# Performance work log

Hardware: AMD Instinct MI355X
Metric: run time of the kernel (lower is better)

The kernel has to match this reference:

```python
import jax, jax.numpy as jnp
import numpy as np

QMAX = 127.0  # 8-bit symmetric: levels in [-128, 127]


def _ste_round(v):
    # round with straight-through estimator (matches torch fake-quant training)
    return v + jax.lax.stop_gradient(jnp.round(v) - v)


def _act_fake_quant(x, clip_factor):
    # per-tensor symmetric fake quant with learnable clip (lac):
    # clip range = sigmoid(clip_factor) * max|x|
    scale = jax.nn.sigmoid(clip_factor) * jnp.max(jnp.abs(x)) / QMAX
    return jnp.clip(_ste_round(x / scale), -QMAX - 1.0, QMAX) * scale


def _weight_fake_quant(w):
    # per-output-channel symmetric fake quant; w: [out, in]
    scale = jnp.max(jnp.abs(w), axis=1, keepdims=True) / QMAX
    return jnp.clip(_ste_round(w / scale), -QMAX - 1.0, QMAX) * scale


def setup_inputs() -> dict:
    key = jax.random.key(0)
    k1, k2, k3, k4 = jax.random.split(key, 4)
    B, S, H, I = 8, 8192, 1024, 2816
    return {
        "x": jax.random.normal(k1, (B, S, H), dtype=jnp.float32),
        "clip_x": jnp.full((1,), 4.0, dtype=jnp.float32),     # sigmoid(4) ~ 0.982
        "clip_down": jnp.full((1,), 4.0, dtype=jnp.float32),
        "w_gate": jax.random.normal(k2, (I, H), dtype=jnp.float32) * 0.02,
        "w_up": jax.random.normal(k3, (I, H), dtype=jnp.float32) * 0.02,
        "w_down": jax.random.normal(k4, (H, I), dtype=jnp.float32) * 0.02,
    }


def reference(x, clip_x, clip_down, w_gate, w_up, w_down):
    # _trans_forward: quantize act -> gate/up quant-matmul -> SwiGLU -> quantize -> down quant-matmul
    xq = _act_fake_quant(x, clip_x[0])                       # [B,S,H]
    gate = jnp.einsum("bsh,ih->bsi", xq, _weight_fake_quant(w_gate))
    up = jnp.einsum("bsh,ih->bsi", xq, _weight_fake_quant(w_up))
    h = _act_fake_quant(jax.nn.silu(gate) * up, clip_down[0])  # [B,S,I]
    return jnp.einsum("bsi,hi->bsh", h, _weight_fake_quant(w_down))
```

## Files before the change

kernel.cpp:

```cpp
#include <hip/hip_runtime.h>
#include <stdint.h>

typedef __attribute__((ext_vector_type(4))) int i32x4;

typedef const __attribute__((address_space(1))) void gvoid_t;
typedef __attribute__((address_space(3))) void lvoid_t;

#define GLD16(g, l) __builtin_amdgcn_global_load_lds((gvoid_t*)(g), (lvoid_t*)(l), 16, 0, 0)
#define FENCE() asm volatile("" ::: "memory")
#define BARRIER() do { FENCE(); __builtin_amdgcn_s_barrier(); FENCE(); } while (0)
#define VMCNT4() asm volatile("s_waitcnt vmcnt(4)" ::: "memory")
#define VMCNT0() asm volatile("s_waitcnt vmcnt(0)" ::: "memory")

__device__ inline int q1mul(float x, float r) {
    return (int)fminf(fmaxf(rintf(x * r), -128.f), 127.f);
}
__device__ inline int q1div(float x, float s) {
    return (int)fminf(fmaxf(rintf(x / s), -128.f), 127.f);
}
__device__ inline int pack4(float4 v, float r) {
    return (q1mul(v.x, r) & 255) | ((q1mul(v.y, r) & 255) << 8) |
           ((q1mul(v.z, r) & 255) << 16) | ((q1mul(v.w, r) & 255) << 24);
}

__global__ void k_absmax(const float* __restrict__ x, size_t n4, unsigned int* __restrict__ out) {
    size_t S = (size_t)gridDim.x * blockDim.x;
    size_t i = (size_t)blockIdx.x * blockDim.x + threadIdx.x;
    const float4* x4 = (const float4*)x;
    float m = 0.f;
    for (; i + 3 * S < n4; i += 4 * S) {
        float4 v0 = x4[i], v1 = x4[i + S], v2 = x4[i + 2 * S], v3 = x4[i + 3 * S];
        m = fmaxf(m, fmaxf(fmaxf(fabsf(v0.x), fabsf(v0.y)), fmaxf(fabsf(v0.z), fabsf(v0.w))));
        m = fmaxf(m, fmaxf(fmaxf(fabsf(v1.x), fabsf(v1.y)), fmaxf(fabsf(v1.z), fabsf(v1.w))));
        m = fmaxf(m, fmaxf(fmaxf(fabsf(v2.x), fabsf(v2.y)), fmaxf(fabsf(v2.z), fabsf(v2.w))));
        m = fmaxf(m, fmaxf(fmaxf(fabsf(v3.x), fabsf(v3.y)), fmaxf(fabsf(v3.z), fabsf(v3.w))));
    }
    for (; i < n4; i += S) {
        float4 v = x4[i];
        m = fmaxf(m, fmaxf(fmaxf(fabsf(v.x), fabsf(v.y)), fmaxf(fabsf(v.z), fabsf(v.w))));
    }
    #pragma unroll
    for (int off = 32; off > 0; off >>= 1) m = fmaxf(m, __shfl_xor(m, off, 64));
    if ((threadIdx.x & 63) == 0) atomicMax(out, __float_as_uint(m));
}

__global__ void k_scale(const float* __restrict__ clip, const unsigned int* __restrict__ maxbits,
                        float* __restrict__ s_out) {
    float m = __uint_as_float(*maxbits);
    float sig = 1.f / (1.f + expf(-clip[0]));
    float s = sig * m / 127.f;
    s_out[0] = s;
    s_out[1] = 1.f / s;
}

__global__ void k_quant_f32_i8(const float* __restrict__ in, int4* __restrict__ out,
                               const float* __restrict__ sptr, size_t n16) {
    float r = sptr[1];
    size_t S = (size_t)gridDim.x * blockDim.x;
    size_t i = (size_t)blockIdx.x * blockDim.x + threadIdx.x;
    const float4* in4 = (const float4*)in;
    for (; i < n16; i += S) {
        float4 v0 = in4[4 * i], v1 = in4[4 * i + 1], v2 = in4[4 * i + 2], v3 = in4[4 * i + 3];
        int4 o;
        o.x = pack4(v0, r); o.y = pack4(v1, r); o.z = pack4(v2, r); o.w = pack4(v3, r);
        out[i] = o;
    }
}

__global__ void k_quant_w_i8(const float* __restrict__ W, int8_t* __restrict__ Q,
                             float* __restrict__ srow, int cols) {
    int row = blockIdx.x;
    const float* w = W + (size_t)row * cols;
    float m = 0.f;
    for (int c = threadIdx.x; c < cols; c += 256) m = fmaxf(m, fabsf(w[c]));
    #pragma unroll
    for (int off = 32; off > 0; off >>= 1) m = fmaxf(m, __shfl_xor(m, off, 64));
    __shared__ float red[4];
    if ((threadIdx.x & 63) == 0) red[threadIdx.x >> 6] = m;
    __syncthreads();
    if (threadIdx.x == 0) {
        float mm = fmaxf(fmaxf(red[0], red[1]), fmaxf(red[2], red[3]));
        red[0] = mm / 127.f;
        srow[row] = mm / 127.f;
    }
    __syncthreads();
    float s = red[0];
    for (int c = threadIdx.x; c < cols; c += 256)
        Q[(size_t)row * cols + c] = (int8_t)q1div(w[c], s);
}

__global__ __launch_bounds__(512, 2) void k_gemm1_i8(
    const int8_t* __restrict__ Aq, const int8_t* __restrict__ Bg, const int8_t* __restrict__ Bu,
    const float* __restrict__ sg, const float* __restrict__ su, const float* __restrict__ sx,
    float* __restrict__ Hout, unsigned int* __restrict__ maxh)
{
    constexpr int K = 1024, N = 2816, NT = K / 128, BUF = 65536;
    __shared__ int8_t lds[2 * BUF];

    const int ntn = N / 128;
    const int chunk = gridDim.x >> 3;
    const int wg = ((int)blockIdx.x & 7) * chunk + ((int)blockIdx.x >> 3);
    const int mt = wg / ntn, nt = wg % ntn;
    const int m0 = mt * 256, n0 = nt * 128;
    const int tid = threadIdx.x;
    const int wid = tid >> 6, lane = tid & 63;
    const int wm = wid >> 2, wn = wid & 3;
    const int lr = lane & 15, lk = lane >> 4;

    const int srow = tid >> 2;
    const int scol = ((tid & 3) ^ ((srow >> 1) & 3)) << 4;
    const int8_t* gA0 = Aq + (size_t)(m0 + srow) * K + scol;
    const int8_t* gA1 = gA0 + (size_t)128 * K;
    const int8_t* gG  = Bg + (size_t)(n0 + srow) * K + scol;
    const int8_t* gU  = Bu + (size_t)(n0 + srow) * K + scol;
    const int ldst = wid << 10;

    const int swz = (lk ^ ((lr >> 1) & 3)) << 4;

    i32x4 accg[8][2] = {};
    i32x4 accu[8][2] = {};

    {
        int8_t* Lw = &lds[0];
        GLD16(gA0,      Lw + ldst);         GLD16(gA1,      Lw + 8192  + ldst);
        GLD16(gG,       Lw + 32768 + ldst); GLD16(gU,       Lw + 40960 + ldst);
        GLD16(gA0 + 64, Lw + 16384 + ldst); GLD16(gA1 + 64, Lw + 24576 + ldst);
        GLD16(gG  + 64, Lw + 49152 + ldst); GLD16(gU  + 64, Lw + 57344 + ldst);
    }
    VMCNT4();
    BARRIER();

    for (int t = 0; t < NT; ++t) {
        const bool st = (t + 1 < NT);
        const size_t kk = (size_t)(t + 1) * 128;
        const int8_t* Lr = &lds[(t & 1) * BUF];
        int8_t* Lw = &lds[((t + 1) & 1) * BUF];
        i32x4 a[4], bg[2], bu[2];

        #pragma unroll
        for (int mi = 0; mi < 4; ++mi)
            a[mi] = *(const i32x4*)(Lr + (wm * 128 + mi * 16 + lr) * 64 + swz);
        #pragma unroll
        for (int ni = 0; ni < 2; ++ni) {
            bg[ni] = *(const i32x4*)(Lr + 32768 + (wn * 32 + ni * 16 + lr) * 64 + swz);
            bu[ni] = *(const i32x4*)(Lr + 40960 + (wn * 32 + ni * 16 + lr) * 64 + swz);
        }
        if (st) { GLD16(gA0 + kk, Lw + ldst); GLD16(gA1 + kk, Lw + 8192 + ldst); }
        BARRIER();
        __builtin_amdgcn_s_setprio(1);
        #pragma unroll
        for (int mi = 0; mi < 4; ++mi)
            #pragma unroll
            for (int ni = 0; ni < 2; ++ni) {
                accg[mi][ni] = __builtin_amdgcn_mfma_i32_16x16x64_i8(a[mi], bg[ni], accg[mi][ni], 0, 0, 0);
                accu[mi][ni] = __builtin_amdgcn_mfma_i32_16x16x64_i8(a[mi], bu[ni], accu[mi][ni], 0, 0, 0);
            }
        __builtin_amdgcn_s_setprio(0);
        BARRIER();

        #pragma unroll
        for (int mi = 0; mi < 4; ++mi)
            a[mi] = *(const i32x4*)(Lr + (wm * 128 + 64 + mi * 16 + lr) * 64 + swz);
        if (st) { GLD16(gG + kk, Lw + 32768 + ldst); GLD16(gU + kk, Lw + 40960 + ldst); }
        BARRIER();
        __builtin_amdgcn_s_setprio(1);
        #pragma unroll
        for (int mi = 0; mi < 4; ++mi)
            #pragma unroll
            for (int ni = 0; ni < 2; ++ni) {
                accg[4 + mi][ni] = __builtin_amdgcn_mfma_i32_16x16x64_i8(a[mi], bg[ni], accg[4 + mi][ni], 0, 0, 0);
                accu[4 + mi][ni] = __builtin_amdgcn_mfma_i32_16x16x64_i8(a[mi], bu[ni], accu[4 + mi][ni], 0, 0, 0);
            }
        __builtin_amdgcn_s_setprio(0);
        if (st) { VMCNT4(); } else { VMCNT0(); }
        BARRIER();

        #pragma unroll
        for (int mi = 0; mi < 4; ++mi)
            a[mi] = *(const i32x4*)(Lr + 16384 + (wm * 128 + mi * 16 + lr) * 64 + swz);
        #pragma unroll
        for (int ni = 0; ni < 2; ++ni) {
            bg[ni] = *(const i32x4*)(Lr + 49152 + (wn * 32 + ni * 16 + lr) * 64 + swz);
            bu[ni] = *(const i32x4*)(Lr + 57344 + (wn * 32 + ni * 16 + lr) * 64 + swz);
        }
        if (st) { GLD16(gA0 + kk + 64, Lw + 16384 + ldst); GLD16(gA1 + kk + 64, Lw + 24576 + ldst); }
        BARRIER();
        __builtin_amdgcn_s_setprio(1);
        #pragma unroll
        for (int mi = 0; mi < 4; ++mi)
            #pragma unroll
            for (int ni = 0; ni < 2; ++ni) {
                accg[mi][ni] = __builtin_amdgcn_mfma_i32_16x16x64_i8(a[mi], bg[ni], accg[mi][ni], 0, 0, 0);
                accu[mi][ni] = __builtin_amdgcn_mfma_i32_16x16x64_i8(a[mi], bu[ni], accu[mi][ni], 0, 0, 0);
            }
        __builtin_amdgcn_s_setprio(0);
        BARRIER();

        #pragma unroll
        for (int mi = 0; mi < 4; ++mi)
            a[mi] = *(const i32x4*)(Lr + 16384 + (wm * 128 + 64 + mi * 16 + lr) * 64 + swz);
        if (st) { GLD16(gG + kk + 64, Lw + 49152 + ldst); GLD16(gU + kk + 64, Lw + 57344 + ldst); }
        BARRIER();
        __builtin_amdgcn_s_setprio(1);
        #pragma unroll
        for (int mi = 0; mi < 4; ++mi)
            #pragma unroll
            for (int ni = 0; ni < 2; ++ni) {
                accg[4 + mi][ni] = __builtin_amdgcn_mfma_i32_16x16x64_i8(a[mi], bg[ni], accg[4 + mi][ni], 0, 0, 0);
                accu[4 + mi][ni] = __builtin_amdgcn_mfma_i32_16x16x64_i8(a[mi], bu[ni], accu[4 + mi][ni], 0, 0, 0);
            }
        __builtin_amdgcn_s_setprio(0);
        if (st) { VMCNT4(); }
        BARRIER();
    }

    const float s_x = sx[0];
    float lmax = 0.f;
    #pragma unroll
    for (int ni = 0; ni < 2; ++ni) {
        const int n = n0 + wn * 32 + ni * 16 + lr;
        const float fg = s_x * sg[n];
        const float fu = s_x * su[n];
        #pragma unroll
        for (int mi = 0; mi < 8; ++mi) {
            const int mb = m0 + wm * 128 + mi * 16 + lk * 4;
            #pragma unroll
            for (int r = 0; r < 4; ++r) {
                float g = (float)accg[mi][ni][r] * fg;
                float u = (float)accu[mi][ni][r] * fu;
                float h = g * u / (1.f + expf(-g));
                Hout[(size_t)(mb + r) * N + n] = h;
                lmax = fmaxf(lmax, fabsf(h));
            }
        }
    }
    #pragma unroll
    for (int off = 32; off > 0; off >>= 1) lmax = fmaxf(lmax, __shfl_xor(lmax, off, 64));
    if (lane == 0) atomicMax(maxh, __float_as_uint(lmax));
}

__global__ __launch_bounds__(512, 2) void k_gemm2_i8(
    const int8_t* __restrict__ Aq, const int8_t* __restrict__ Bw,
    const float* __restrict__ sw, const float* __restrict__ sh,
    float* __restrict__ Out)
{
    constexpr int K = 2816, N = 1024, NT = K / 128, BUF = 65536;
    __shared__ int8_t lds[2 * BUF];

    const int chunk = gridDim.x >> 3;
    const int wg = ((int)blockIdx.x & 7) * chunk + ((int)blockIdx.x >> 3);
    const int mt = wg >> 2, nt = wg & 3;
    const int m0 = mt * 256, n0 = nt * 256;
    const int tid = threadIdx.x;
    const int wid = tid >> 6, lane = tid & 63;
    const int wm = wid >> 2, wn = wid & 3;
    const int lr = lane & 15, lk = lane >> 4;

    const int srow = tid >> 2;
    const int scol = ((tid & 3) ^ ((srow >> 1) & 3)) << 4;
    const int8_t* gA0 = Aq + (size_t)(m0 + srow) * K + scol;
    const int8_t* gA1 = gA0 + (size_t)128 * K;
    const int8_t* gB0 = Bw + (size_t)(n0 + srow) * K + scol;
    const int8_t* gB1 = gB0 + (size_t)128 * K;
    const int ldst = wid << 10;

    const int swz = (lk ^ ((lr >> 1) & 3)) << 4;

    i32x4 acc[8][4] = {};

    {
        int8_t* Lw = &lds[0];
        GLD16(gA0,      Lw + ldst);         GLD16(gA1,      Lw + 8192  + ldst);
        GLD16(gB0,      Lw + 32768 + ldst); GLD16(gB1,      Lw + 40960 + ldst);
        GLD16(gA0 + 64, Lw + 16384 + ldst); GLD16(gA1 + 64, Lw + 24576 + ldst);
        GLD16(gB0 + 64, Lw + 49152 + ldst); GLD16(gB1 + 64, Lw + 57344 + ldst);
    }
    VMCNT4();
    BARRIER();

    for (int t = 0; t < NT; ++t) {
        const bool st = (t + 1 < NT);
        const size_t kk = (size_t)(t + 1) * 128;
        const int8_t* Lr = &lds[(t & 1) * BUF];
        int8_t* Lw = &lds[((t + 1) & 1) * BUF];
        i32x4 a[4], b[4];

        #pragma unroll
        for (int mi = 0; mi < 4; ++mi)
            a[mi] = *(const i32x4*)(Lr + (wm * 128 + mi * 16 + lr) * 64 + swz);
        #pragma unroll
        for (int ni = 0; ni < 4; ++ni)
            b[ni] = *(const i32x4*)(Lr + 32768 + (wn * 64 + ni * 16 + lr) * 64 + swz);
        if (st) { GLD16(gA0 + kk, Lw + ldst); GLD16(gA1 + kk, Lw + 8192 + ldst); }
        BARRIER();
        __builtin_amdgcn_s_setprio(1);
        #pragma unroll
        for (int mi = 0; mi < 4; ++mi)
            #pragma unroll
            for (int ni = 0; ni < 4; ++ni)
                acc[mi][ni] = __builtin_amdgcn_mfma_i32_16x16x64_i8(a[mi], b[ni], acc[mi][ni], 0, 0, 0);
        __builtin_amdgcn_s_setprio(0);
        BARRIER();

        #pragma unroll
        for (int mi = 0; mi < 4; ++mi)
            a[mi] = *(const i32x4*)(Lr + (wm * 128 + 64 + mi * 16 + lr) * 64 + swz);
        if (st) { GLD16(gB0 + kk, Lw + 32768 + ldst); GLD16(gB1 + kk, Lw + 40960 + ldst); }
        BARRIER();
        __builtin_amdgcn_s_setprio(1);
        #pragma unroll
        for (int mi = 0; mi < 4; ++mi)
            #pragma unroll
            for (int ni = 0; ni < 4; ++ni)
                acc[4 + mi][ni] = __builtin_amdgcn_mfma_i32_16x16x64_i8(a[mi], b[ni], acc[4 + mi][ni], 0, 0, 0);
        __builtin_amdgcn_s_setprio(0);
        if (st) { VMCNT4(); } else { VMCNT0(); }
        BARRIER();

        #pragma unroll
        for (int mi = 0; mi < 4; ++mi)
            a[mi] = *(const i32x4*)(Lr + 16384 + (wm * 128 + mi * 16 + lr) * 64 + swz);
        #pragma unroll
        for (int ni = 0; ni < 4; ++ni)
            b[ni] = *(const i32x4*)(Lr + 49152 + (wn * 64 + ni * 16 + lr) * 64 + swz);
        if (st) { GLD16(gA0 + kk + 64, Lw + 16384 + ldst); GLD16(gA1 + kk + 64, Lw + 24576 + ldst); }
        BARRIER();
        __builtin_amdgcn_s_setprio(1);
        #pragma unroll
        for (int mi = 0; mi < 4; ++mi)
            #pragma unroll
            for (int ni = 0; ni < 4; ++ni)
                acc[mi][ni] = __builtin_amdgcn_mfma_i32_16x16x64_i8(a[mi], b[ni], acc[mi][ni], 0, 0, 0);
        __builtin_amdgcn_s_setprio(0);
        BARRIER();

        #pragma unroll
        for (int mi = 0; mi < 4; ++mi)
            a[mi] = *(const i32x4*)(Lr + 16384 + (wm * 128 + 64 + mi * 16 + lr) * 64 + swz);
        if (st) { GLD16(gB0 + kk + 64, Lw + 49152 + ldst); GLD16(gB1 + kk + 64, Lw + 57344 + ldst); }
        BARRIER();
        __builtin_amdgcn_s_setprio(1);
        #pragma unroll
        for (int mi = 0; mi < 4; ++mi)
            #pragma unroll
            for (int ni = 0; ni < 4; ++ni)
                acc[4 + mi][ni] = __builtin_amdgcn_mfma_i32_16x16x64_i8(a[mi], b[ni], acc[4 + mi][ni], 0, 0, 0);
        __builtin_amdgcn_s_setprio(0);
        if (st) { VMCNT4(); }
        BARRIER();
    }

    const float s_h = sh[0];
    #pragma unroll
    for (int ni = 0; ni < 4; ++ni) {
        const int n = n0 + wn * 64 + ni * 16 + lr;
        const float f = s_h * sw[n];
        #pragma unroll
        for (int mi = 0; mi < 8; ++mi) {
            const int mb = m0 + wm * 128 + mi * 16 + lk * 4;
            #pragma unroll
            for (int r = 0; r < 4; ++r)
                Out[(size_t)(mb + r) * N + n] = (float)acc[mi][ni][r] * f;
        }
    }
}

extern "C" void kernel_launch(void* const* d_in, const int* in_sizes, int n_in,
                              void* d_out, int out_size, void* d_ws, size_t ws_size,
                              hipStream_t stream) {
    const float* x       = (const float*)d_in[0];
    const float* clip_x  = (const float*)d_in[1];
    const float* clip_dn = (const float*)d_in[2];
    const float* w_gate  = (const float*)d_in[3];
    const float* w_up    = (const float*)d_in[4];
    const float* w_down  = (const float*)d_in[5];
    float* out = (float*)d_out;

    const int Hd = 1024, Id = 2816;
    const int M = in_sizes[0] / Hd;
    const size_t nx = (size_t)M * Hd;
    const size_t nh = (size_t)M * Id;

    char* ws = (char*)d_ws;
    size_t off = 0;
    auto alloc = [&](size_t bytes) -> char* {
        char* p = ws + off;
        off = (off + bytes + 255) & ~(size_t)255;
        return p;
    };
    unsigned int* max_slots = (unsigned int*)alloc(8);
    float* sxp = (float*)alloc(8);
    float* shp = (float*)alloc(8);
    int8_t* qx  = (int8_t*)alloc(nx);
    int8_t* qwg = (int8_t*)alloc((size_t)Id * Hd);
    int8_t* qwu = (int8_t*)alloc((size_t)Id * Hd);
    int8_t* qwd = (int8_t*)alloc((size_t)Hd * Id);
    float* swg = (float*)alloc((size_t)Id * 4);
    float* swu = (float*)alloc((size_t)Id * 4);
    float* swd = (float*)alloc((size_t)Hd * 4);
    int8_t* qh = (int8_t*)alloc(nh);
    float* hbuf = (float*)alloc(nh * 4);

    hipMemsetAsync(max_slots, 0, 8, stream);

    k_absmax<<<4096, 256, 0, stream>>>(x, nx / 4, &max_slots[0]);
    k_scale<<<1, 1, 0, stream>>>(clip_x, &max_slots[0], sxp);
    k_quant_f32_i8<<<2048, 256, 0, stream>>>(x, (int4*)qx, sxp, nx / 16);
    k_quant_w_i8<<<Id, 256, 0, stream>>>(w_gate, qwg, swg, Hd);
    k_quant_w_i8<<<Id, 256, 0, stream>>>(w_up, qwu, swu, Hd);
    k_quant_w_i8<<<Hd, 256, 0, stream>>>(w_down, qwd, swd, Id);

    k_gemm1_i8<<<(M / 256) * (Id / 128), 512, 0, stream>>>(qx, qwg, qwu, swg, swu, sxp,
                                                           hbuf, &max_slots[1]);
    k_scale<<<1, 1, 0, stream>>>(clip_dn, &max_slots[1], shp);
    k_quant_f32_i8<<<4096, 256, 0, stream>>>(hbuf, (int4*)qh, shp, nh / 16);

    k_gemm2_i8<<<(M / 256) * (Hd / 256), 512, 0, stream>>>(qh, qwd, swd, shp, out);
}
```

Before: 1.372 ms.

## Store SwiGLU intermediate as per-block-scaled int16 and split gemm1 into two launches

The gate/up GEMM epilogue now reduces a per-tile absmax, then writes the SwiGLU output as int16 scaled by that tile max instead of fp32, halving intermediate write and read traffic. A new requantization kernel rescales the int16 values to int8 using the per-block scale and the global clip scale. Gemm1 is split into two launches over the two halves of the N tiles, with a new XCD-aware tile mapping. The epilogue recomputes SiLU twice and adds a block barrier. The int16 intermediate adds a small extra rounding step before the int8 quantization.

```diff
diff --git a/kernel.cpp b/kernel.cpp
--- a/kernel.cpp
+++ b/kernel.cpp
@@ -67,6 +67,32 @@
     }
 }
 
+__global__ void k_quant_h16_i8(const short* __restrict__ h16, const float* __restrict__ sblk,
+                               const float* __restrict__ sh, int4* __restrict__ qh, size_t nchunks) {
+    const float rh = sh[1] * (1.f / 32766.f);
+    size_t S = (size_t)gridDim.x * blockDim.x;
+    size_t i = (size_t)blockIdx.x * blockDim.x + threadIdx.x;
+    for (; i < nchunks; i += S) {
+        int row = (int)(i / 176);
+        int col = (int)(i - (size_t)row * 176) * 16;
+        float f = sblk[(row >> 8) * 22 + (col >> 7)] * rh;
+        const int4* p = (const int4*)(h16 + (size_t)row * 2816 + col);
+        int4 lo = p[0], hi = p[1];
+        int w[8] = {lo.x, lo.y, lo.z, lo.w, hi.x, hi.y, hi.z, hi.w};
+        int ob[4];
+        #pragma unroll
+        for (int j = 0; j < 4; ++j) {
+            int q0 = q1mul((float)(short)(w[2 * j] & 0xFFFF), f);
+            int q1 = q1mul((float)(short)(w[2 * j] >> 16), f);
+            int q2 = q1mul((float)(short)(w[2 * j + 1] & 0xFFFF), f);
+            int q3 = q1mul((float)(short)(w[2 * j + 1] >> 16), f);
+            ob[j] = (q0 & 255) | ((q1 & 255) << 8) | ((q2 & 255) << 16) | ((q3 & 255) << 24);
+        }
+        int4 o; o.x = ob[0]; o.y = ob[1]; o.z = ob[2]; o.w = ob[3];
+        qh[i] = o;
+    }
+}
+
 __global__ void k_quant_w_i8(const float* __restrict__ W, int8_t* __restrict__ Q,
                              float* __restrict__ srow, int cols) {
     int row = blockIdx.x;
@@ -92,15 +118,17 @@
 __global__ __launch_bounds__(512, 2) void k_gemm1_i8(
     const int8_t* __restrict__ Aq, const int8_t* __restrict__ Bg, const int8_t* __restrict__ Bu,
     const float* __restrict__ sg, const float* __restrict__ su, const float* __restrict__ sx,
-    float* __restrict__ Hout, unsigned int* __restrict__ maxh)
+    short* __restrict__ H16, float* __restrict__ sblk, unsigned int* __restrict__ maxh,
+    int nt_base)
 {
     constexpr int K = 1024, N = 2816, NT = K / 128, BUF = 65536;
     __shared__ int8_t lds[2 * BUF];
 
-    const int ntn = N / 128;
-    const int chunk = gridDim.x >> 3;
-    const int wg = ((int)blockIdx.x & 7) * chunk + ((int)blockIdx.x >> 3);
-    const int mt = wg / ntn, nt = wg % ntn;
+    const int wgl = (int)blockIdx.x >> 3;
+    const int xcd = (int)blockIdx.x & 7;
+    const int mtspan = (int)(gridDim.x >> 3) / 11;
+    const int mt = xcd * mtspan + wgl / 11;
+    const int nt = nt_base + wgl % 11;
     const int m0 = mt * 256, n0 = nt * 128;
     const int tid = threadIdx.x;
     const int wid = tid >> 6, lane = tid & 63;
@@ -223,20 +251,45 @@
         const float fu = s_x * su[n];
         #pragma unroll
         for (int mi = 0; mi < 8; ++mi) {
-            const int mb = m0 + wm * 128 + mi * 16 + lk * 4;
             #pragma unroll
             for (int r = 0; r < 4; ++r) {
                 float g = (float)accg[mi][ni][r] * fg;
                 float u = (float)accu[mi][ni][r] * fu;
                 float h = g * u / (1.f + expf(-g));
-                Hout[(size_t)(mb + r) * N + n] = h;
                 lmax = fmaxf(lmax, fabsf(h));
             }
         }
     }
     #pragma unroll
     for (int off = 32; off > 0; off >>= 1) lmax = fmaxf(lmax, __shfl_xor(lmax, off, 64));
-    if (lane == 0) atomicMax(maxh, __float_as_uint(lmax));
+    float* lred = (float*)lds;
+    if (lane == 0) lred[wid] = lmax;
+    BARRIER();
+    float bmax = lred[0];
+    #pragma unroll
+    for (int w = 1; w < 8; ++w) bmax = fmaxf(bmax, lred[w]);
+    if (tid == 0) {
+        atomicMax(maxh, __float_as_uint(bmax));
+        sblk[mt * 22 + nt] = bmax;
+    }
+    const float qs = 32766.f / fmaxf(bmax, 1e-20f);
+    #pragma unroll
+    for (int ni = 0; ni < 2; ++ni) {
+        const int n = n0 + wn * 32 + ni * 16 + lr;
+        const float fg = s_x * sg[n];
+        const float fu = s_x * su[n];
+        #pragma unroll
+        for (int mi = 0; mi < 8; ++mi) {
+            const int mb = m0 + wm * 128 + mi * 16 + lk * 4;
+            #pragma unroll
+            for (int r = 0; r < 4; ++r) {
+                float g = (float)accg[mi][ni][r] * fg;
+                float u = (float)accu[mi][ni][r] * fu;
+                float h = g * u / (1.f + expf(-g));
+                H16[(size_t)(mb + r) * N + n] = (short)rintf(h * qs);
+            }
+        }
+    }
 }
 
 __global__ __launch_bounds__(512, 2) void k_gemm2_i8(
@@ -399,7 +452,8 @@
     float* swu = (float*)alloc((size_t)Id * 4);
     float* swd = (float*)alloc((size_t)Hd * 4);
     int8_t* qh = (int8_t*)alloc(nh);
-    float* hbuf = (float*)alloc(nh * 4);
+    short* h16 = (short*)alloc(nh * 2);
+    float* sblk = (float*)alloc((size_t)(M / 256) * 22 * 4);
 
     hipMemsetAsync(max_slots, 0, 8, stream);
 
@@ -410,10 +464,11 @@
     k_quant_w_i8<<<Id, 256, 0, stream>>>(w_up, qwu, swu, Hd);
     k_quant_w_i8<<<Hd, 256, 0, stream>>>(w_down, qwd, swd, Id);
 
-    k_gemm1_i8<<<(M / 256) * (Id / 128), 512, 0, stream>>>(qx, qwg, qwu, swg, swu, sxp,
-                                                           hbuf, &max_slots[1]);
+    const int g1grid = (M / 256) * 11;
+    k_gemm1_i8<<<g1grid, 512, 0, stream>>>(qx, qwg, qwu, swg, swu, sxp, h16, sblk, &max_slots[1], 0);
+    k_gemm1_i8<<<g1grid, 512, 0, stream>>>(qx, qwg, qwu, swg, swu, sxp, h16, sblk, &max_slots[1], 11);
     k_scale<<<1, 1, 0, stream>>>(clip_dn, &max_slots[1], shp);
-    k_quant_f32_i8<<<4096, 256, 0, stream>>>(hbuf, (int4*)qh, shp, nh / 16);
+    k_quant_h16_i8<<<4096, 256, 0, stream>>>(h16, sblk, shp, (int4*)qh, nh / 16);
 
     k_gemm2_i8<<<(M / 256) * (Hd / 256), 512, 0, stream>>>(qh, qwd, swd, shp, out);
 }
```

New measurement: 1.258 ms. 8.4% less time.
